# Kernel tuning notes

Measured on AMD Instinct MI355X. Metric: run time of the kernel, lower is better.

## Reference

```python
import jax, jax.numpy as jnp
import numpy as np


def to_float8(x, exp_bits=4, mant_bits=3):
    # Faithful port of the torch to_float8: clamp exponent, round mantissa.
    max_exp = 2 ** (exp_bits - 1) - 1
    scale = 2.0 ** mant_bits
    sign = jnp.sign(x)
    xa = jnp.abs(x)
    e = jnp.clip(jnp.floor(jnp.log2(xa + 1e-08)), -max_exp, max_exp)
    p = jnp.exp2(e)
    mant_q = jnp.round((xa / p - 1.0) * scale) / scale
    return sign * (1.0 + mant_q) * p


def setup_inputs() -> dict:
    key = jax.random.key(0)
    k0, k1, k2, k3, k4 = jax.random.split(key, 5)
    Bz, Din, L, N, Dout = 32, 512, 512, 512, 512
    u = jax.random.normal(k0, (Bz, Din, L), jnp.float32)
    # |A| < 1 for a stable length-512 recurrence
    A_diag = jax.random.uniform(k1, (N,), jnp.float32, 0.0, 0.9)
    B = jax.random.normal(k2, (N, Din), jnp.float32) * (1.0 / np.sqrt(Din))
    C = jax.random.normal(k3, (Dout, N), jnp.float32) * (1.0 / np.sqrt(N))
    D = jax.random.normal(k4, (Dout, Din), jnp.float32) * (1.0 / np.sqrt(Din))
    return {"u": u, "A_diag": A_diag, "B": B, "C": C, "D": D}


def reference(u, A_diag, B, C, D):
    int_bits, mant_bits = 4, 3
    q = lambda t: to_float8(t, int_bits, mant_bits)
    A_q = q(A_diag)[None, :]          # [1, N]
    B_q, C_q, D_q = q(B), q(C), q(D)
    Bt = B_q.T                         # [Din, N]
    # row_checksum(B_q.t()): append column of row sums -> constant across steps
    right_cs = jnp.concatenate([Bt, Bt.sum(axis=1, keepdims=True)], axis=1)  # [Din, N+1]
    Bz, Din, L = u.shape
    N = A_diag.shape[0]
    u_t = jnp.transpose(u, (2, 0, 1))  # [L, Bz, Din]

    def step(state, ut):
        # col_checksum(ut): append row of column sums
        left_cs = jnp.concatenate([ut, ut.sum(axis=0, keepdims=True)], axis=0)  # [Bz+1, Din]
        prod_cs = left_cs @ right_cs                 # [Bz+1, N+1] checksum-padded matmul
        right_term = prod_cs[:-1, :-1]               # ut @ B_q.T  (ABFT mask is discarded in forward)
        state_q = q(state * A_q + right_term)        # [Bz, N]
        y = q(state_q @ C_q.T + ut @ D_q.T)          # [Bz, Dout]
        return state_q, y

    state0 = jnp.zeros((Bz, N), u.dtype)
    _, Y = jax.lax.scan(step, state0, u_t)           # [L, Bz, Dout]
    return jnp.transpose(Y, (1, 2, 0))               # [Bz, Dout, L]
```

## Files before the change

### kernel.cpp

```cpp
#include <hip/hip_runtime.h>
#include <hip/hip_bf16.h>


#define DINX 512
#define LSEQ 512
#define NDIM 512

__device__ __forceinline__ float q8(float x) {
    float xa = fabsf(x);
    float w  = __fadd_rn(xa, 1e-8f);
    int e = (int)((__float_as_uint(w) >> 23) & 0xFFu) - 127;
    e = e < -7 ? -7 : (e > 7 ? 7 : e);
    float p    = __int_as_float((unsigned)((e + 127) << 23));
    float invp = __int_as_float((unsigned)((127 - e) << 23));
    float t  = __fmul_rn(__fsub_rn(__fmul_rn(xa, invp), 1.0f), 8.0f);
    float m  = __fmul_rn(rintf(t), 0.125f);
    float r  = __fmul_rn(__fadd_rn(1.0f, m), p);
    return copysignf(r, x);
}

__global__ __launch_bounds__(256) void quantT3A(const float* __restrict__ B,
                                                const float* __restrict__ C,
                                                const float* __restrict__ D,
                                                const float* __restrict__ A,
                                                float* __restrict__ Bqt,
                                                float* __restrict__ Cqt,
                                                float* __restrict__ Dqt,
                                                float* __restrict__ Aq) {
    __shared__ float tl[32][33];
    if (blockIdx.z == 0 && blockIdx.x == 0 && blockIdx.y == 0) {
        Aq[threadIdx.x]       = q8(A[threadIdx.x]);
        Aq[256 + threadIdx.x] = q8(A[256 + threadIdx.x]);
    }
    const float* in = blockIdx.z == 0 ? B : (blockIdx.z == 1 ? C : D);
    float* out      = blockIdx.z == 0 ? Bqt : (blockIdx.z == 1 ? Cqt : Dqt);
    const int r0 = blockIdx.y * 32, c0 = blockIdx.x * 32;
    const int x = threadIdx.x & 31, y = threadIdx.x >> 5;
#pragma unroll
    for (int i = 0; i < 32; i += 8)
        tl[y + i][x] = q8(in[(r0 + y + i) * 512 + c0 + x]);
    __syncthreads();
#pragma unroll
    for (int i = 0; i < 32; i += 8)
        out[(c0 + y + i) * 512 + r0 + x] = tl[x][y + i];
}

__device__ __forceinline__ void gemm_pass(const float* __restrict__ X,
                                          const float* __restrict__ W,
                                          int m0, int n0, int KTOT,
                                          float (&acc)[2][4][2][4],
                                          float (*Xs)[128], float (*Ws)[128],
                                          int tid) {
    const int tx = tid & 15, ty = tid >> 4;
    const int srow = tid >> 4, sseg4 = (tid & 15) * 4;
    const float* xp = X + (size_t)srow * 512 + m0 + sseg4;
    const float* wp = W + (size_t)srow * 512 + n0 + sseg4;
    for (int k0 = 0; k0 < KTOT; k0 += 32) {
        float4 x0 = *(const float4*)xp;
        float4 x1 = *(const float4*)(xp + 64);
        float4 x2 = *(const float4*)(xp + 16 * 512);
        float4 x3 = *(const float4*)(xp + 16 * 512 + 64);
        float4 w0 = *(const float4*)wp;
        float4 w1 = *(const float4*)(wp + 64);
        float4 w2 = *(const float4*)(wp + 16 * 512);
        float4 w3 = *(const float4*)(wp + 16 * 512 + 64);
        xp += 32 * 512; wp += 32 * 512;
        __syncthreads();
        *(float4*)&Xs[srow][sseg4]           = x0;
        *(float4*)&Xs[srow][64 + sseg4]      = x1;
        *(float4*)&Xs[16 + srow][sseg4]      = x2;
        *(float4*)&Xs[16 + srow][64 + sseg4] = x3;
        *(float4*)&Ws[srow][sseg4]           = w0;
        *(float4*)&Ws[srow][64 + sseg4]      = w1;
        *(float4*)&Ws[16 + srow][sseg4]      = w2;
        *(float4*)&Ws[16 + srow][64 + sseg4] = w3;
        __syncthreads();
#pragma unroll
        for (int k = 0; k < 32; ++k) {
            float a[2][4], b[2][4];
            *(float4*)&a[0][0] = *(const float4*)&Xs[k][tx * 4];
            *(float4*)&a[1][0] = *(const float4*)&Xs[k][64 + tx * 4];
            *(float4*)&b[0][0] = *(const float4*)&Ws[k][ty * 4];
            *(float4*)&b[1][0] = *(const float4*)&Ws[k][64 + ty * 4];
#pragma unroll
            for (int p = 0; p < 2; ++p)
#pragma unroll
                for (int i = 0; i < 4; ++i)
#pragma unroll
                    for (int q = 0; q < 2; ++q)
#pragma unroll
                        for (int j = 0; j < 4; ++j)
                            acc[p][i][q][j] = fmaf(a[p][i], b[q][j], acc[p][i][q][j]);
        }
    }
}

__global__ __launch_bounds__(256, 4) void gemm_RD(const float* __restrict__ u,
                                                  const float* __restrict__ Bqt,
                                                  const float* __restrict__ Dqt,
                                                  float* __restrict__ R,
                                                  float* __restrict__ Pd) {
    __shared__ float Xs[32][128];
    __shared__ float Ws[32][128];
    const int zz = blockIdx.z;
    const int b  = zz & 31;
    const bool isR = zz < 32;
    const int t0 = blockIdx.x * 128, n0 = blockIdx.y * 128;
    const int tid = threadIdx.x;
    const int tx = tid & 15, ty = tid >> 4;
    const float* ub = u + (size_t)b * (DINX * LSEQ);
    const float* Wm = isR ? Bqt : Dqt;
    float acc[2][4][2][4] = {};
    gemm_pass(ub, Wm, t0, n0, DINX, acc, Xs, Ws, tid);
    if (isR) {
        float* Rb = R + (size_t)b * (LSEQ * NDIM);
#pragma unroll
        for (int p = 0; p < 2; ++p)
#pragma unroll
            for (int i = 0; i < 4; ++i) {
                float* row = Rb + (size_t)(t0 + p * 64 + tx * 4 + i) * NDIM + n0;
                *(float4*)(row + ty * 4)      = make_float4(acc[p][i][0][0], acc[p][i][0][1],
                                                            acc[p][i][0][2], acc[p][i][0][3]);
                *(float4*)(row + 64 + ty * 4) = make_float4(acc[p][i][1][0], acc[p][i][1][1],
                                                            acc[p][i][1][2], acc[p][i][1][3]);
            }
    } else {
        float* Yb = Pd + (size_t)b * (NDIM * LSEQ);
#pragma unroll
        for (int q = 0; q < 2; ++q)
#pragma unroll
            for (int j = 0; j < 4; ++j) {
                float* row = Yb + (size_t)(n0 + q * 64 + ty * 4 + j) * LSEQ + t0;
                *(float4*)(row + tx * 4)      = make_float4(acc[0][0][q][j], acc[0][1][q][j],
                                                            acc[0][2][q][j], acc[0][3][q][j]);
                *(float4*)(row + 64 + tx * 4) = make_float4(acc[1][0][q][j], acc[1][1][q][j],
                                                            acc[1][2][q][j], acc[1][3][q][j]);
            }
    }
}

__global__ __launch_bounds__(64) void recur(const float* __restrict__ R,
                                            const float* __restrict__ Aq,
                                            float* __restrict__ S) {
    __shared__ float tile[16][68];
    const int b  = blockIdx.x;
    const int n0 = blockIdx.y * 64;
    const int n  = threadIdx.x;
    const float a = Aq[n0 + n];
    const float* Rb = R + (size_t)b * (LSEQ * NDIM) + n0;
    float* Sb = S + (size_t)b * (NDIM * LSEQ) + (size_t)n0 * LSEQ;
    float s = 0.0f;
    const int c = (n & 3) * 4;
    const int rbase = n >> 2;
    for (int t0 = 0; t0 < LSEQ; t0 += 16) {
#pragma unroll
        for (int tt = 0; tt < 16; ++tt) {
            float r = Rb[(size_t)(t0 + tt) * NDIM + n];
            s = q8(__fadd_rn(__fmul_rn(s, a), r));
            tile[tt][n] = s;
        }
        __syncthreads();
#pragma unroll
        for (int p = 0; p < 4; ++p) {
            int row = p * 16 + rbase;
            float4 v = make_float4(tile[c + 0][row], tile[c + 1][row],
                                   tile[c + 2][row], tile[c + 3][row]);
            *(float4*)(Sb + (size_t)row * LSEQ + t0 + c) = v;
        }
        __syncthreads();
    }
}

__global__ __launch_bounds__(256) void gemm_YC(const float* __restrict__ S,
                                               const float* __restrict__ Cqt,
                                               float* __restrict__ Y) {
    __shared__ float Xs[32][128];
    __shared__ float Ws[32][128];
    const int b  = blockIdx.z;
    const int t0 = blockIdx.x * 128, o0 = blockIdx.y * 128;
    const int tid = threadIdx.x;
    const int tx = tid & 15, ty = tid >> 4;
    const float* Sb = S + (size_t)b * (NDIM * LSEQ);
    float acc[2][4][2][4] = {};
    gemm_pass(Sb, Cqt, t0, o0, NDIM, acc, Xs, Ws, tid);

    float* Yb = Y + (size_t)b * (NDIM * LSEQ);
#pragma unroll
    for (int q = 0; q < 2; ++q)
#pragma unroll
        for (int j = 0; j < 4; ++j) {
            float* row = Yb + (size_t)(o0 + q * 64 + ty * 4 + j) * LSEQ + t0;
            float4 v0 = *(const float4*)(row + tx * 4);
            float4 v1 = *(const float4*)(row + 64 + tx * 4);
            *(float4*)(row + tx * 4) =
                make_float4(q8(__fadd_rn(acc[0][0][q][j], v0.x)),
                            q8(__fadd_rn(acc[0][1][q][j], v0.y)),
                            q8(__fadd_rn(acc[0][2][q][j], v0.z)),
                            q8(__fadd_rn(acc[0][3][q][j], v0.w)));
            *(float4*)(row + 64 + tx * 4) =
                make_float4(q8(__fadd_rn(acc[1][0][q][j], v1.x)),
                            q8(__fadd_rn(acc[1][1][q][j], v1.y)),
                            q8(__fadd_rn(acc[1][2][q][j], v1.z)),
                            q8(__fadd_rn(acc[1][3][q][j], v1.w)));
        }
}

extern "C" void kernel_launch(void* const* d_in, const int* in_sizes, int n_in,
                              void* d_out, int out_size, void* d_ws, size_t ws_size,
                              hipStream_t stream) {
    const float* u = (const float*)d_in[0];
    const float* A = (const float*)d_in[1];
    const float* B = (const float*)d_in[2];
    const float* C = (const float*)d_in[3];
    const float* D = (const float*)d_in[4];

    float* ws  = (float*)d_ws;
    float* Aq  = ws;
    float* Bqt = Aq + 512;
    float* Cqt = Bqt + 262144;
    float* Dqt = Cqt + 262144;
    float* R   = Dqt + 262144;
    float* S   = R + 8388608;
    float* Y   = (float*)d_out;

    quantT3A<<<dim3(16, 16, 3), 256, 0, stream>>>(B, C, D, A, Bqt, Cqt, Dqt, Aq);
    gemm_RD<<<dim3(4, 4, 64), 256, 0, stream>>>(u, Bqt, Dqt, R, Y);
    recur<<<dim3(32, 8), 64, 0, stream>>>(R, Aq, S);
    gemm_YC<<<dim3(4, 4, 32), 256, 0, stream>>>(S, Cqt, Y);
}
```

Before: 393.3 us.

## Overlap D-projection GEMM with the recurrence and C/D quantization with R GEMM

Restructures the launch schedule. The quantization of C and D now runs in the same grid as the u·Bqᵀ GEMM, and the u·Dqᵀ GEMM is moved into the same grid as the sequential recurrence. The recurrence uses only 256 blocks of 64 active threads, so running the D GEMM beside it is meant to fill idle compute units during that latency-bound phase. The cost is that recurrence blocks now occupy 256-thread slots with 192 idle threads, and the GEMM blocks run at lower occupancy because of the launch bound of 3.

```diff
diff --git a/kernel.cpp b/kernel.cpp
--- a/kernel.cpp
+++ b/kernel.cpp
@@ -1,5 +1,4 @@
 #include <hip/hip_runtime.h>
-#include <hip/hip_bf16.h>
 
 
 #define DINX 512
@@ -19,30 +18,24 @@
     return copysignf(r, x);
 }
 
-__global__ __launch_bounds__(256) void quantT3A(const float* __restrict__ B,
-                                                const float* __restrict__ C,
-                                                const float* __restrict__ D,
-                                                const float* __restrict__ A,
-                                                float* __restrict__ Bqt,
-                                                float* __restrict__ Cqt,
-                                                float* __restrict__ Dqt,
-                                                float* __restrict__ Aq) {
+__global__ __launch_bounds__(256) void quantBA(const float* __restrict__ B,
+                                               const float* __restrict__ A,
+                                               float* __restrict__ Bqt,
+                                               float* __restrict__ Aq) {
     __shared__ float tl[32][33];
-    if (blockIdx.z == 0 && blockIdx.x == 0 && blockIdx.y == 0) {
+    if (blockIdx.x == 0 && blockIdx.y == 0) {
         Aq[threadIdx.x]       = q8(A[threadIdx.x]);
         Aq[256 + threadIdx.x] = q8(A[256 + threadIdx.x]);
     }
-    const float* in = blockIdx.z == 0 ? B : (blockIdx.z == 1 ? C : D);
-    float* out      = blockIdx.z == 0 ? Bqt : (blockIdx.z == 1 ? Cqt : Dqt);
     const int r0 = blockIdx.y * 32, c0 = blockIdx.x * 32;
     const int x = threadIdx.x & 31, y = threadIdx.x >> 5;
 #pragma unroll
     for (int i = 0; i < 32; i += 8)
-        tl[y + i][x] = q8(in[(r0 + y + i) * 512 + c0 + x]);
+        tl[y + i][x] = q8(B[(r0 + y + i) * 512 + c0 + x]);
     __syncthreads();
 #pragma unroll
     for (int i = 0; i < 32; i += 8)
-        out[(c0 + y + i) * 512 + r0 + x] = tl[x][y + i];
+        Bqt[(c0 + y + i) * 512 + r0 + x] = tl[x][y + i];
 }
 
 __device__ __forceinline__ void gemm_pass(const float* __restrict__ X,
@@ -95,24 +88,24 @@
     }
 }
 
-__global__ __launch_bounds__(256, 4) void gemm_RD(const float* __restrict__ u,
-                                                  const float* __restrict__ Bqt,
-                                                  const float* __restrict__ Dqt,
-                                                  float* __restrict__ R,
-                                                  float* __restrict__ Pd) {
-    __shared__ float Xs[32][128];
-    __shared__ float Ws[32][128];
-    const int zz = blockIdx.z;
-    const int b  = zz & 31;
-    const bool isR = zz < 32;
-    const int t0 = blockIdx.x * 128, n0 = blockIdx.y * 128;
+__global__ __launch_bounds__(256, 4) void fused_RqCD(const float* __restrict__ u,
+                                                     const float* __restrict__ Bqt,
+                                                     const float* __restrict__ C,
+                                                     const float* __restrict__ D,
+                                                     float* __restrict__ R,
+                                                     float* __restrict__ Cqt,
+                                                     float* __restrict__ Dqt) {
+    __shared__ float ldsbuf[2 * 32 * 128];
+    const int zz = blockIdx.x;
     const int tid = threadIdx.x;
-    const int tx = tid & 15, ty = tid >> 4;
-    const float* ub = u + (size_t)b * (DINX * LSEQ);
-    const float* Wm = isR ? Bqt : Dqt;
-    float acc[2][4][2][4] = {};
-    gemm_pass(ub, Wm, t0, n0, DINX, acc, Xs, Ws, tid);
-    if (isR) {
+    if (zz < 512) {
+        float (*Xs)[128] = (float(*)[128])ldsbuf;
+        float (*Ws)[128] = (float(*)[128])(ldsbuf + 32 * 128);
+        const int b = zz & 31, t0 = ((zz >> 5) & 3) * 128, n0 = (zz >> 7) * 128;
+        const int tx = tid & 15, ty = tid >> 4;
+        const float* ub = u + (size_t)b * (DINX * LSEQ);
+        float acc[2][4][2][4] = {};
+        gemm_pass(ub, Bqt, t0, n0, DINX, acc, Xs, Ws, tid);
         float* Rb = R + (size_t)b * (LSEQ * NDIM);
 #pragma unroll
         for (int p = 0; p < 2; ++p)
@@ -125,49 +118,84 @@
                                                             acc[p][i][1][2], acc[p][i][1][3]);
             }
     } else {
+        float (*tl)[33] = (float(*)[33])ldsbuf;
+        const int d = zz - 512;
+        const float* in = (d >> 8) ? D : C;
+        float* out      = (d >> 8) ? Dqt : Cqt;
+        const int c0 = (d & 15) * 32, r0 = ((d >> 4) & 15) * 32;
+        const int x = tid & 31, y = tid >> 5;
+#pragma unroll
+        for (int i = 0; i < 32; i += 8)
+            tl[y + i][x] = q8(in[(r0 + y + i) * 512 + c0 + x]);
+        __syncthreads();
+#pragma unroll
+        for (int i = 0; i < 32; i += 8)
+            out[(c0 + y + i) * 512 + r0 + x] = tl[x][y + i];
+    }
+}
+
+__global__ __launch_bounds__(256, 3) void fused_Drec(const float* __restrict__ u,
+                                                     const float* __restrict__ Dqt,
+                                                     const float* __restrict__ R,
+                                                     const float* __restrict__ Aq,
+                                                     float* __restrict__ Pd,
+                                                     float* __restrict__ S) {
+    __shared__ float ldsbuf[2 * 32 * 128];
+    const int zz = blockIdx.x;
+    const int tid = threadIdx.x;
+    if (zz >= 256) {
+        float (*Xs)[128] = (float(*)[128])ldsbuf;
+        float (*Ws)[128] = (float(*)[128])(ldsbuf + 32 * 128);
+        const int d = zz - 256;
+        const int b = d & 31, t0 = ((d >> 5) & 3) * 128, o0 = (d >> 7) * 128;
+        const int tx = tid & 15, ty = tid >> 4;
+        const float* ub = u + (size_t)b * (DINX * LSEQ);
+        float acc[2][4][2][4] = {};
+        gemm_pass(ub, Dqt, t0, o0, DINX, acc, Xs, Ws, tid);
         float* Yb = Pd + (size_t)b * (NDIM * LSEQ);
 #pragma unroll
         for (int q = 0; q < 2; ++q)
 #pragma unroll
             for (int j = 0; j < 4; ++j) {
-                float* row = Yb + (size_t)(n0 + q * 64 + ty * 4 + j) * LSEQ + t0;
+                float* row = Yb + (size_t)(o0 + q * 64 + ty * 4 + j) * LSEQ + t0;
                 *(float4*)(row + tx * 4)      = make_float4(acc[0][0][q][j], acc[0][1][q][j],
                                                             acc[0][2][q][j], acc[0][3][q][j]);
                 *(float4*)(row + 64 + tx * 4) = make_float4(acc[1][0][q][j], acc[1][1][q][j],
                                                             acc[1][2][q][j], acc[1][3][q][j]);
             }
-    }
-}
-
-__global__ __launch_bounds__(64) void recur(const float* __restrict__ R,
-                                            const float* __restrict__ Aq,
-                                            float* __restrict__ S) {
-    __shared__ float tile[16][68];
-    const int b  = blockIdx.x;
-    const int n0 = blockIdx.y * 64;
-    const int n  = threadIdx.x;
-    const float a = Aq[n0 + n];
-    const float* Rb = R + (size_t)b * (LSEQ * NDIM) + n0;
-    float* Sb = S + (size_t)b * (NDIM * LSEQ) + (size_t)n0 * LSEQ;
-    float s = 0.0f;
-    const int c = (n & 3) * 4;
-    const int rbase = n >> 2;
-    for (int t0 = 0; t0 < LSEQ; t0 += 16) {
-#pragma unroll
-        for (int tt = 0; tt < 16; ++tt) {
-            float r = Rb[(size_t)(t0 + tt) * NDIM + n];
-            s = q8(__fadd_rn(__fmul_rn(s, a), r));
-            tile[tt][n] = s;
+    } else {
+        float (*tile)[68] = (float(*)[68])ldsbuf;
+        const int b  = zz >> 3;
+        const int n0 = (zz & 7) * 64;
+        const int n  = tid & 63;
+        const bool act = tid < 64;
+        float a = 0.0f, s = 0.0f;
+        const float* Rb = R + (size_t)b * (LSEQ * NDIM) + n0;
+        float* Sb = S + (size_t)b * (NDIM * LSEQ) + (size_t)n0 * LSEQ;
+        if (act) a = Aq[n0 + n];
+        const int c = (n & 3) * 4;
+        const int rbase = n >> 2;
+        for (int t0 = 0; t0 < LSEQ; t0 += 16) {
+            if (act) {
+#pragma unroll
+                for (int tt = 0; tt < 16; ++tt) {
+                    float r = Rb[(size_t)(t0 + tt) * NDIM + n];
+                    s = q8(__fadd_rn(__fmul_rn(s, a), r));
+                    tile[tt][n] = s;
+                }
+            }
+            __syncthreads();
+            if (act) {
+#pragma unroll
+                for (int p = 0; p < 4; ++p) {
+                    int row = p * 16 + rbase;
+                    float4 v = make_float4(tile[c + 0][row], tile[c + 1][row],
+                                           tile[c + 2][row], tile[c + 3][row]);
+                    *(float4*)(Sb + (size_t)row * LSEQ + t0 + c) = v;
+                }
+            }
+            __syncthreads();
         }
-        __syncthreads();
-#pragma unroll
-        for (int p = 0; p < 4; ++p) {
-            int row = p * 16 + rbase;
-            float4 v = make_float4(tile[c + 0][row], tile[c + 1][row],
-                                   tile[c + 2][row], tile[c + 3][row]);
-            *(float4*)(Sb + (size_t)row * LSEQ + t0 + c) = v;
-        }
-        __syncthreads();
     }
 }
 
@@ -223,8 +251,8 @@
     float* S   = R + 8388608;
     float* Y   = (float*)d_out;
 
-    quantT3A<<<dim3(16, 16, 3), 256, 0, stream>>>(B, C, D, A, Bqt, Cqt, Dqt, Aq);
-    gemm_RD<<<dim3(4, 4, 64), 256, 0, stream>>>(u, Bqt, Dqt, R, Y);
-    recur<<<dim3(32, 8), 64, 0, stream>>>(R, Aq, S);
+    quantBA<<<dim3(16, 16), 256, 0, stream>>>(B, A, Bqt, Aq);
+    fused_RqCD<<<1024, 256, 0, stream>>>(u, Bqt, C, D, R, Cqt, Dqt);
+    fused_Drec<<<768, 256, 0, stream>>>(u, Dqt, R, Aq, Y, S);
     gemm_YC<<<dim3(4, 4, 32), 256, 0, stream>>>(S, Cqt, Y);
 }
```

Measured after the change: 372.8 us (median of 2 runs). -5.2%, faster.
